# Kernel tuning notes

Hardware: AMD Instinct MI355X
Metric: run time of the kernel (lower is better)

## Reference

```python
import jax, jax.numpy as jnp
import numpy as np

N_NODES = 50000


def _gcn_layer(x, src, dst, W, b, n_nodes):
    # PyG GCNConv: h = x @ W, add self-loops, sym-normalized scatter-add, + bias
    h = x @ W  # [N, Dout]
    loop = jnp.arange(n_nodes, dtype=src.dtype)
    src2 = jnp.concatenate([src, loop])
    dst2 = jnp.concatenate([dst, loop])
    ones = jnp.ones(src2.shape[0], dtype=x.dtype)
    deg = jax.ops.segment_sum(ones, dst2, num_segments=n_nodes)  # in-degree w/ self-loops
    dinv = jnp.where(deg > 0, jax.lax.rsqrt(deg), 0.0)
    norm = dinv[src2] * dinv[dst2]  # [E+N]
    msg = h[src2] * norm[:, None]   # gather + scale
    out = jax.ops.segment_sum(msg, dst2, num_segments=n_nodes)  # scatter-add
    return out + b


def setup_inputs() -> dict:
    key = jax.random.key(0)
    k1, k2, k3, k4 = jax.random.split(key, 4)
    x = jax.random.normal(k1, (N_NODES, 128), dtype=jnp.float32)
    edge_index = jax.random.randint(k2, (2, 500000), 0, N_NODES, dtype=jnp.int64)
    W1 = jax.random.normal(k3, (128, 128), dtype=jnp.float32) * (1.0 / np.sqrt(128))
    b1 = jnp.zeros((128,), dtype=jnp.float32)
    W2 = jax.random.normal(k4, (128, 64), dtype=jnp.float32) * (1.0 / np.sqrt(128))
    b2 = jnp.zeros((64,), dtype=jnp.float32)
    return {"x": x, "edge_index": edge_index, "W1": W1, "b1": b1, "W2": W2, "b2": b2}


def reference(x, edge_index, W1, b1, W2, b2):
    src, dst = edge_index[0], edge_index[1]
    n = x.shape[0]
    h = _gcn_layer(x, src, dst, W1, b1, n)
    h = jax.nn.relu(h)
    out = _gcn_layer(h, src, dst, W2, b2, n)
    return out
```

## Files before the change

### kernel.cpp

```cpp
#include <hip/hip_runtime.h>
#include <hip/hip_bf16.h>
#include <cstddef>


typedef __attribute__((ext_vector_type(8))) short short8;
typedef __attribute__((ext_vector_type(4))) float f32x4;
typedef unsigned long long u64;

__device__ inline unsigned short f2bf(float f) {
    __hip_bfloat16 b = __float2bfloat16(f);
    return *reinterpret_cast<unsigned short*>(&b);
}
__device__ inline float bf2f_lo(unsigned int u) {
    unsigned int v = u << 16;
    return *reinterpret_cast<float*>(&v);
}
__device__ inline float bf2f_hi(unsigned int u) {
    unsigned int v = u & 0xffff0000u;
    return *reinterpret_cast<float*>(&v);
}
__device__ inline u64 ld_acq64(u64* p) {
    return __hip_atomic_load(p, __ATOMIC_ACQUIRE, __HIP_MEMORY_SCOPE_AGENT);
}
__device__ inline void st_rel64(u64* p, u64 v) {
    __hip_atomic_store(p, v, __ATOMIC_RELEASE, __HIP_MEMORY_SCOPE_AGENT);
}

__global__ __launch_bounds__(256) void count_kernel(const int* __restrict__ dst, int E,
                                                    int* __restrict__ deg,
                                                    unsigned short* __restrict__ rank,
                                                    const float* __restrict__ W1,
                                                    const float* __restrict__ W2,
                                                    unsigned short* __restrict__ W1f,
                                                    unsigned short* __restrict__ W2f,
                                                    u64* __restrict__ lb, int CB) {
    int b = blockIdx.x;
    int tid = threadIdx.x;
    if (b >= CB) {
        int idx = (b - CB) * 256 + tid;
        if (idx < 64) lb[idx] = 0;
        if (idx < 3072) {
            const float* W;
            unsigned short* Wf;
            int n, oct, Nc;
            if (idx < 2048) { W = W1; Wf = W1f; Nc = 128; n = idx >> 4; oct = idx & 15; }
            else { W = W2; Wf = W2f; Nc = 64; int i2 = idx - 2048; n = i2 >> 4; oct = i2 & 15; }
            int k0 = oct * 8;
            int ks = k0 >> 5, quad = (k0 >> 3) & 3, ntg = n >> 4;
            short8 v;
            #pragma unroll
            for (int j = 0; j < 8; j++) v[j] = (short)f2bf(W[(k0 + j) * Nc + n]);
            int off = (((ntg * 4 + ks) * 64) + (n & 15) + 16 * quad) * 8;
            *(short8*)(Wf + off) = v;
        }
        return;
    }
    int i = (b * 256 + tid) * 4;
    if (i + 3 < E) {
        int4 d = *(const int4*)(dst + i);
        unsigned short r0 = (unsigned short)atomicAdd(&deg[d.x], 1);
        unsigned short r1 = (unsigned short)atomicAdd(&deg[d.y], 1);
        unsigned short r2 = (unsigned short)atomicAdd(&deg[d.z], 1);
        unsigned short r3 = (unsigned short)atomicAdd(&deg[d.w], 1);
        *(ushort4*)(rank + i) = make_ushort4(r0, r1, r2, r3);
    } else {
        for (; i < E; i++) rank[i] = (unsigned short)atomicAdd(&deg[dst[i]], 1);
    }
}

__global__ __launch_bounds__(256) void scan_lb_kernel(const int* __restrict__ deg, int N,
                                                      u64* __restrict__ lb,
                                                      int* __restrict__ offs,
                                                      float* __restrict__ dinv) {
    __shared__ int ws[4];
    __shared__ int s_prefix;
    int tid = threadIdx.x;
    int sb = blockIdx.x;
    int SB = gridDim.x;
    int lane = tid & 63;
    int wv = tid >> 6;

    int i = sb * 1024 + tid * 4;
    int v0 = (i + 0 < N) ? deg[i + 0] : 0;
    int v1 = (i + 1 < N) ? deg[i + 1] : 0;
    int v2 = (i + 2 < N) ? deg[i + 2] : 0;
    int v3 = (i + 3 < N) ? deg[i + 3] : 0;
    int tsum = v0 + v1 + v2 + v3;
    int xs = tsum;
    #pragma unroll
    for (int off = 1; off < 64; off <<= 1) {
        int y = __shfl_up(xs, off, 64);
        if (lane >= off) xs += y;
    }
    if (lane == 63) ws[wv] = xs;
    __syncthreads();
    int wprefix = 0;
    #pragma unroll
    for (int w2 = 0; w2 < 4; w2++) wprefix += (w2 < wv) ? ws[w2] : 0;
    int chunk_total = ws[0] + ws[1] + ws[2] + ws[3];

    if (wv == 0) {
        if (lane == 0)
            st_rel64(&lb[sb], ((u64)(unsigned)chunk_total << 2) | 1ull);
        int contrib = 0;
        if (sb > 0) {
            int pred = sb - 1 - lane;
            for (;;) {
                u64 v = (pred >= 0) ? ld_acq64(&lb[pred]) : 2ull;
                int flag = (int)(v & 3);
                u64 ball2 = __ballot(flag == 2);
                u64 ball0 = __ballot(flag == 0);
                if (ball2 != 0) {
                    int L = __ffsll(ball2) - 1;
                    if ((ball0 & ((1ull << L) - 1)) == 0) {
                        contrib = (lane <= L) ? (int)(unsigned)(v >> 2) : 0;
                        break;
                    }
                }
                __builtin_amdgcn_s_sleep(1);
            }
            #pragma unroll
            for (int off = 32; off >= 1; off >>= 1)
                contrib += __shfl_xor(contrib, off, 64);
        }
        if (lane == 0) {
            st_rel64(&lb[sb], ((u64)(unsigned)(contrib + chunk_total) << 2) | 2ull);
            s_prefix = contrib;
        }
    }
    __syncthreads();

    int carry = s_prefix;
    int e0 = carry + wprefix + xs - tsum;
    int e1 = e0 + v0, e2 = e1 + v1, e3 = e2 + v2;
    if (i + 0 < N) { offs[i + 0] = e0; dinv[i + 0] = rsqrtf((float)(v0 + 1)); }
    if (i + 1 < N) { offs[i + 1] = e1; dinv[i + 1] = rsqrtf((float)(v1 + 1)); }
    if (i + 2 < N) { offs[i + 2] = e2; dinv[i + 2] = rsqrtf((float)(v2 + 1)); }
    if (i + 3 < N) { offs[i + 3] = e3; dinv[i + 3] = rsqrtf((float)(v3 + 1)); }
    if (sb == SB - 1 && tid == 0) offs[N] = carry + chunk_total;
}

__global__ __launch_bounds__(256) void fillgemm_kernel(
    const float* __restrict__ x, const unsigned short* __restrict__ W1f,
    unsigned short* __restrict__ h1, int N,
    const int* __restrict__ src, const int* __restrict__ dst, int E,
    const int* __restrict__ offs, const unsigned short* __restrict__ rank,
    const float* __restrict__ dinv, int* __restrict__ csr) {

    const int FB = (E + 255) / 256;
    int b = blockIdx.x;
    int tid = threadIdx.x;

    __shared__ unsigned short As[64 * 128];
    __shared__ float sdinv[64];

    if (b < FB) {
        int i = b * 256 + tid;
        if (i < E) {
            int s = src[i];
            int d = dst[i];
            int pos = offs[d] + (int)rank[i];
            csr[pos] = s;
        }
        return;
    }

    constexpr int K = 128, BN = 128;
    int lane = tid & 63;
    int w = tid >> 6;
    int row0 = (b - FB) * 64;

    if (tid < 64) {
        int gr = row0 + tid;
        sdinv[tid] = (gr < N) ? dinv[gr] : 0.f;
    }

    short8 bfr[2][4];
    #pragma unroll
    for (int nl = 0; nl < 2; nl++)
        #pragma unroll
        for (int ks = 0; ks < 4; ks++)
            bfr[nl][ks] = *(const short8*)(W1f + ((((w * 2 + nl) * 4 + ks) * 64) + lane) * 8);

    #pragma unroll
    for (int it = 0; it < 8; it++) {
        int idx = it * 256 + tid;
        int row = idx >> 5, kq = idx & 31;
        int k0 = kq * 4;
        int ks = k0 >> 5, quad = (k0 >> 3) & 3, j0 = k0 & 7, mt = row >> 4;
        ushort4 o = make_ushort4(0, 0, 0, 0);
        int gr = row0 + row;
        if (gr < N) {
            float4 a = *(const float4*)(x + (size_t)gr * K + k0);
            o.x = f2bf(a.x); o.y = f2bf(a.y); o.z = f2bf(a.z); o.w = f2bf(a.w);
        }
        int off = (((mt * 4 + ks) * 64) + (row & 15) + 16 * quad) * 8 + j0;
        *(ushort4*)(As + off) = o;
    }
    __syncthreads();

    f32x4 acc[4][2];
    #pragma unroll
    for (int mt = 0; mt < 4; mt++)
        #pragma unroll
        for (int nl = 0; nl < 2; nl++) acc[mt][nl] = (f32x4){0.f, 0.f, 0.f, 0.f};

    #pragma unroll
    for (int ks = 0; ks < 4; ks++) {
        short8 af[4];
        #pragma unroll
        for (int mt = 0; mt < 4; mt++)
            af[mt] = *(const short8*)(As + (((mt * 4 + ks) * 64) + lane) * 8);
        #pragma unroll
        for (int mt = 0; mt < 4; mt++)
            #pragma unroll
            for (int nl = 0; nl < 2; nl++)
                acc[mt][nl] = __builtin_amdgcn_mfma_f32_16x16x32_bf16(
                    af[mt], bfr[nl][ks], acc[mt][nl], 0, 0, 0);
    }

    int col16 = lane & 15;
    int rowq = lane >> 4;
    #pragma unroll
    for (int mt = 0; mt < 4; mt++) {
        #pragma unroll
        for (int nl = 0; nl < 2; nl++) {
            int gc = (w * 2 + nl) * 16 + col16;
            #pragma unroll
            for (int r = 0; r < 4; r++) {
                int lr = mt * 16 + rowq * 4 + r;
                int gr = row0 + lr;
                if (gr < N) h1[(size_t)gr * BN + gc] = f2bf(acc[mt][nl][r] * sdinv[lr]);
            }
        }
    }
}

__global__ __launch_bounds__(256) void aggmm_kernel(const unsigned short* __restrict__ h1,
                                                    const int* __restrict__ offs,
                                                    const int* __restrict__ csr,
                                                    const float* __restrict__ dinv,
                                                    const float* __restrict__ b1,
                                                    const unsigned short* __restrict__ W2f,
                                                    unsigned short* __restrict__ h2,
                                                    int n) {
    __shared__ unsigned short As[4 * 64 * 8];

    int tid = threadIdx.x;
    int t = tid & 63;
    int w = tid >> 6;
    int p = t >> 5;
    int t5 = t & 31;
    int nodebase = blockIdx.x * 16;
    int node0 = nodebase + w * 4;

    int ov = offs[min(node0 + min(t, 4), n)];
    int e0a[4], dega[4], cidx[4];
    #pragma unroll
    for (int i = 0; i < 4; i++) {
        e0a[i] = __shfl(ov, i, 64);
        int e1v = __shfl(ov, i + 1, 64);
        dega[i] = e1v - e0a[i];
        int ce = e0a[i] + min(t, max(dega[i] - 1, 0));
        cidx[i] = (dega[i] > 0) ? csr[ce] : 0;
    }

    short8 bw[4];
    #pragma unroll
    for (int ks = 0; ks < 4; ks++)
        bw[ks] = *(const short8*)(W2f + (((w * 4 + ks) * 64) + t) * 8);

    float4 bias = *(const float4*)(b1 + t5 * 4);

    #pragma unroll
    for (int i = 0; i < 4; i++) {
        int row16 = w * 4 + i;
        int node = node0 + i;
        float a0 = 0.f, a1 = 0.f, a2 = 0.f, a3 = 0.f;
        float di = 0.f;
        int deg = dega[i];
        int nb = min(deg, 64);
        if (node < n) {
            di = dinv[node];
            if (p == 0) {
                uint2 su = *(const uint2*)(h1 + (size_t)node * 128 + t5 * 4);
                a0 = bf2f_lo(su.x); a1 = bf2f_hi(su.x);
                a2 = bf2f_lo(su.y); a3 = bf2f_hi(su.y);
            }
            for (int jb = 0; jb < nb; jb += 8) {
                #pragma unroll
                for (int j = 0; j < 4; j++) {
                    int ee = jb + j * 2 + p;
                    int ec = min(ee, nb - 1);
                    int s = __shfl(cidx[i], ec, 64);
                    float wgt = (ee < deg) ? 1.f : 0.f;
                    uint2 hu = *(const uint2*)(h1 + (size_t)s * 128 + t5 * 4);
                    a0 += bf2f_lo(hu.x) * wgt; a1 += bf2f_hi(hu.x) * wgt;
                    a2 += bf2f_lo(hu.y) * wgt; a3 += bf2f_hi(hu.y) * wgt;
                }
            }
            int e1 = e0a[i] + deg;
            for (int eb = e0a[i] + 64; eb < e1; eb += 8) {
                #pragma unroll
                for (int j = 0; j < 4; j++) {
                    int ee = eb + j * 2 + p;
                    int ec = min(ee, e1 - 1);
                    int s = csr[ec];
                    float wgt = (ee < e1) ? 1.f : 0.f;
                    uint2 hu = *(const uint2*)(h1 + (size_t)s * 128 + t5 * 4);
                    a0 += bf2f_lo(hu.x) * wgt; a1 += bf2f_hi(hu.x) * wgt;
                    a2 += bf2f_lo(hu.y) * wgt; a3 += bf2f_hi(hu.y) * wgt;
                }
            }
        }
        a0 += __shfl_xor(a0, 32, 64);
        a1 += __shfl_xor(a1, 32, 64);
        a2 += __shfl_xor(a2, 32, 64);
        a3 += __shfl_xor(a3, 32, 64);
        if (p == 0) {
            if (node < n) {
                a0 = fmaxf(a0 * di + bias.x, 0.f);
                a1 = fmaxf(a1 * di + bias.y, 0.f);
                a2 = fmaxf(a2 * di + bias.z, 0.f);
                a3 = fmaxf(a3 * di + bias.w, 0.f);
            }
            int k0 = t5 * 4;
            int ks = k0 >> 5, quad = (k0 >> 3) & 3, j0 = k0 & 7;
            ushort4 pk4 = make_ushort4(f2bf(a0), f2bf(a1), f2bf(a2), f2bf(a3));
            *(ushort4*)(As + ((ks * 64) + row16 + 16 * quad) * 8 + j0) = pk4;
        }
    }
    __syncthreads();

    f32x4 acc = (f32x4){0.f, 0.f, 0.f, 0.f};
    #pragma unroll
    for (int ks = 0; ks < 4; ks++) {
        short8 af = *(const short8*)(As + ((ks * 64) + t) * 8);
        acc = __builtin_amdgcn_mfma_f32_16x16x32_bf16(af, bw[ks], acc, 0, 0, 0);
    }

    int col = w * 16 + (t & 15);
    int rowq = t >> 4;
    #pragma unroll
    for (int r = 0; r < 4; r++) {
        int gr = nodebase + rowq * 4 + r;
        if (gr < n) h2[(size_t)gr * 64 + col] = f2bf(acc[r] * dinv[gr]);
    }
}

__global__ __launch_bounds__(256) void aggout_kernel(const unsigned short* __restrict__ h2,
                                                     const int* __restrict__ offs,
                                                     const int* __restrict__ csr,
                                                     const float* __restrict__ dinv,
                                                     const float* __restrict__ b2,
                                                     float* __restrict__ out, int n) {
    int tid = threadIdx.x;
    int t = tid & 63;
    int w = tid >> 6;
    int node = blockIdx.x * 4 + w;
    if (node >= n) return;
    int p = t >> 4;
    int t4 = t & 15;

    int e0 = offs[node];
    int e1 = offs[node + 1];
    int deg = e1 - e0;
    int nb = min(deg, 64);
    int cidx = (deg > 0) ? csr[e0 + min(t, max(deg - 1, 0))] : 0;

    float a0 = 0.f, a1 = 0.f, a2 = 0.f, a3 = 0.f;
    float di = dinv[node];
    if (p == 0) {
        uint2 su = *(const uint2*)(h2 + (size_t)node * 64 + t4 * 4);
        a0 = bf2f_lo(su.x); a1 = bf2f_hi(su.x);
        a2 = bf2f_lo(su.y); a3 = bf2f_hi(su.y);
    }

    for (int jb = 0; jb < nb; jb += 8) {
        #pragma unroll
        for (int j = 0; j < 2; j++) {
            int ee = jb + j * 4 + p;
            int ec = min(ee, nb - 1);
            int s = __shfl(cidx, ec, 64);
            float wgt = (ee < deg) ? 1.f : 0.f;
            uint2 hu = *(const uint2*)(h2 + (size_t)s * 64 + t4 * 4);
            a0 += bf2f_lo(hu.x) * wgt; a1 += bf2f_hi(hu.x) * wgt;
            a2 += bf2f_lo(hu.y) * wgt; a3 += bf2f_hi(hu.y) * wgt;
        }
    }
    for (int eb = e0 + 64; eb < e1; eb += 8) {
        #pragma unroll
        for (int j = 0; j < 2; j++) {
            int ee = eb + j * 4 + p;
            int ec = min(ee, e1 - 1);
            int s = csr[ec];
            float wgt = (ee < e1) ? 1.f : 0.f;
            uint2 hu = *(const uint2*)(h2 + (size_t)s * 64 + t4 * 4);
            a0 += bf2f_lo(hu.x) * wgt; a1 += bf2f_hi(hu.x) * wgt;
            a2 += bf2f_lo(hu.y) * wgt; a3 += bf2f_hi(hu.y) * wgt;
        }
    }
    a0 += __shfl_xor(a0, 16, 64); a1 += __shfl_xor(a1, 16, 64);
    a2 += __shfl_xor(a2, 16, 64); a3 += __shfl_xor(a3, 16, 64);
    a0 += __shfl_xor(a0, 32, 64); a1 += __shfl_xor(a1, 32, 64);
    a2 += __shfl_xor(a2, 32, 64); a3 += __shfl_xor(a3, 32, 64);
    if (p == 0) {
        float4 bb = *(const float4*)(b2 + t4 * 4);
        *(float4*)(out + (size_t)node * 64 + t4 * 4) =
            make_float4(a0 * di + bb.x, a1 * di + bb.y, a2 * di + bb.z, a3 * di + bb.w);
    }
}

extern "C" void kernel_launch(void* const* d_in, const int* in_sizes, int n_in,
                              void* d_out, int out_size, void* d_ws, size_t ws_size,
                              hipStream_t stream) {
    const float* x  = (const float*)d_in[0];
    const int*   ei = (const int*)d_in[1];
    const float* W1 = (const float*)d_in[2];
    const float* b1 = (const float*)d_in[3];
    const float* W2 = (const float*)d_in[4];
    const float* b2 = (const float*)d_in[5];

    const int N = in_sizes[0] / 128;
    const int E = in_sizes[1] / 2;
    const int* src = ei;
    const int* dst = ei + E;

    char* p = (char*)d_ws;
    auto alloc = [&](size_t bytes) {
        char* r = p;
        p += (bytes + 255) & ~(size_t)255;
        return r;
    };
    int*   degi  = (int*)  alloc((size_t)N * 4);
    float* dinv  = (float*)alloc((size_t)N * 4);
    int*   offs  = (int*)  alloc((size_t)(N + 1) * 4);
    u64*   lb    = (u64*)  alloc((size_t)64 * 8);
    unsigned short* rank = (unsigned short*)alloc((size_t)E * 2);
    int*            csr  = (int*)alloc((size_t)E * 4);
    unsigned short* W1f  = (unsigned short*)alloc((size_t)128 * 128 * 2);
    unsigned short* W2f  = (unsigned short*)alloc((size_t)64 * 128 * 2);
    unsigned short* h1   = (unsigned short*)alloc((size_t)N * 128 * 2);
    unsigned short* h2   = (unsigned short*)alloc((size_t)N * 64 * 2);
    float* out = (float*)d_out;

    const int GB = (N + 63) / 64;
    const int FB = (E + 255) / 256;
    const int SB = (N + 1023) / 1024;
    const int CB = (E / 4 + 255) / 256;

    hipMemsetAsync(degi, 0, (size_t)N * 4, stream);
    count_kernel<<<CB + 12, 256, 0, stream>>>(dst, E, degi, rank,
                                              W1, W2, W1f, W2f, lb, CB);
    scan_lb_kernel<<<SB, 256, 0, stream>>>(degi, N, lb, offs, dinv);
    fillgemm_kernel<<<FB + GB, 256, 0, stream>>>(x, W1f, h1, N, src, dst, E,
                                                 offs, rank, dinv, csr);
    aggmm_kernel<<<(N + 15) / 16, 256, 0, stream>>>(h1, offs, csr, dinv, b1, W2f, h2, N);
    aggout_kernel<<<(N + 3) / 4, 256, 0, stream>>>(h2, offs, csr, dinv, b2, out, N);
}
```

Measured before the change: 171.2 us.

## Restructure GCN pipeline: fuse GEMM with degree count, per-edge weights, interleaved aggregation

Replaces the memset with an init kernel and moves the first GEMM into the degree-count kernel. The GEMM no longer depends on dinv, so it runs alongside the atomics instead of after the scan. The source-side normalization is now stored per edge in a csrw array written during CSR fill, and layer-1 aggregation applies it per edge. Both aggregation kernels now interleave edges from four nodes per wave to expose more memory parallelism. The cost is an extra E-sized float array plus its gather and store, and more registers per thread.

```diff
diff --git a/kernel.cpp b/kernel.cpp
--- a/kernel.cpp
+++ b/kernel.cpp
@@ -26,45 +26,127 @@
     __hip_atomic_store(p, v, __ATOMIC_RELEASE, __HIP_MEMORY_SCOPE_AGENT);
 }
 
-__global__ __launch_bounds__(256) void count_kernel(const int* __restrict__ dst, int E,
-                                                    int* __restrict__ deg,
-                                                    unsigned short* __restrict__ rank,
-                                                    const float* __restrict__ W1,
-                                                    const float* __restrict__ W2,
-                                                    unsigned short* __restrict__ W1f,
-                                                    unsigned short* __restrict__ W2f,
-                                                    u64* __restrict__ lb, int CB) {
+__global__ __launch_bounds__(256) void init_kernel(int* __restrict__ deg, int N,
+                                                   const float* __restrict__ W1,
+                                                   const float* __restrict__ W2,
+                                                   unsigned short* __restrict__ W1f,
+                                                   unsigned short* __restrict__ W2f,
+                                                   u64* __restrict__ lb, int ZB) {
     int b = blockIdx.x;
     int tid = threadIdx.x;
-    if (b >= CB) {
-        int idx = (b - CB) * 256 + tid;
-        if (idx < 64) lb[idx] = 0;
-        if (idx < 3072) {
-            const float* W;
-            unsigned short* Wf;
-            int n, oct, Nc;
-            if (idx < 2048) { W = W1; Wf = W1f; Nc = 128; n = idx >> 4; oct = idx & 15; }
-            else { W = W2; Wf = W2f; Nc = 64; int i2 = idx - 2048; n = i2 >> 4; oct = i2 & 15; }
-            int k0 = oct * 8;
-            int ks = k0 >> 5, quad = (k0 >> 3) & 3, ntg = n >> 4;
-            short8 v;
+    if (b < ZB) {
+        int i = (b * 256 + tid) * 4;
+        if (i + 3 < N) *(int4*)(deg + i) = make_int4(0, 0, 0, 0);
+        else for (; i < N; i++) deg[i] = 0;
+        return;
+    }
+    int idx = (b - ZB) * 256 + tid;
+    if (idx < 64) lb[idx] = 0;
+    if (idx < 3072) {
+        const float* W;
+        unsigned short* Wf;
+        int n, oct, Nc;
+        if (idx < 2048) { W = W1; Wf = W1f; Nc = 128; n = idx >> 4; oct = idx & 15; }
+        else { W = W2; Wf = W2f; Nc = 64; int i2 = idx - 2048; n = i2 >> 4; oct = i2 & 15; }
+        int k0 = oct * 8;
+        int ks = k0 >> 5, quad = (k0 >> 3) & 3, ntg = n >> 4;
+        short8 v;
+        #pragma unroll
+        for (int j = 0; j < 8; j++) v[j] = (short)f2bf(W[(k0 + j) * Nc + n]);
+        int off = (((ntg * 4 + ks) * 64) + (n & 15) + 16 * quad) * 8;
+        *(short8*)(Wf + off) = v;
+    }
+}
+
+__global__ __launch_bounds__(256) void countgemm_kernel(
+    const int* __restrict__ dst, int E,
+    int* __restrict__ deg, unsigned short* __restrict__ rank,
+    const float* __restrict__ x, const unsigned short* __restrict__ W1f,
+    unsigned short* __restrict__ h1, int N, int CB) {
+
+    int b = blockIdx.x;
+    int tid = threadIdx.x;
+
+    __shared__ unsigned short As[64 * 128];
+
+    if (b < CB) {
+        int i = (b * 256 + tid) * 4;
+        if (i + 3 < E) {
+            int4 d = *(const int4*)(dst + i);
+            unsigned short r0 = (unsigned short)atomicAdd(&deg[d.x], 1);
+            unsigned short r1 = (unsigned short)atomicAdd(&deg[d.y], 1);
+            unsigned short r2 = (unsigned short)atomicAdd(&deg[d.z], 1);
+            unsigned short r3 = (unsigned short)atomicAdd(&deg[d.w], 1);
+            *(ushort4*)(rank + i) = make_ushort4(r0, r1, r2, r3);
+        } else {
+            for (; i < E; i++) rank[i] = (unsigned short)atomicAdd(&deg[dst[i]], 1);
+        }
+        return;
+    }
+
+    constexpr int K = 128, BN = 128;
+    int lane = tid & 63;
+    int w = tid >> 6;
+    int row0 = (b - CB) * 64;
+
+    short8 bfr[2][4];
+    #pragma unroll
+    for (int nl = 0; nl < 2; nl++)
+        #pragma unroll
+        for (int ks = 0; ks < 4; ks++)
+            bfr[nl][ks] = *(const short8*)(W1f + ((((w * 2 + nl) * 4 + ks) * 64) + lane) * 8);
+
+    #pragma unroll
+    for (int it = 0; it < 8; it++) {
+        int idx = it * 256 + tid;
+        int row = idx >> 5, kq = idx & 31;
+        int k0 = kq * 4;
+        int ks = k0 >> 5, quad = (k0 >> 3) & 3, j0 = k0 & 7, mt = row >> 4;
+        ushort4 o = make_ushort4(0, 0, 0, 0);
+        int gr = row0 + row;
+        if (gr < N) {
+            float4 a = *(const float4*)(x + (size_t)gr * K + k0);
+            o.x = f2bf(a.x); o.y = f2bf(a.y); o.z = f2bf(a.z); o.w = f2bf(a.w);
+        }
+        int off = (((mt * 4 + ks) * 64) + (row & 15) + 16 * quad) * 8 + j0;
+        *(ushort4*)(As + off) = o;
+    }
+    __syncthreads();
+
+    f32x4 acc[4][2];
+    #pragma unroll
+    for (int mt = 0; mt < 4; mt++)
+        #pragma unroll
+        for (int nl = 0; nl < 2; nl++) acc[mt][nl] = (f32x4){0.f, 0.f, 0.f, 0.f};
+
+    #pragma unroll
+    for (int ks = 0; ks < 4; ks++) {
+        short8 af[4];
+        #pragma unroll
+        for (int mt = 0; mt < 4; mt++)
+            af[mt] = *(const short8*)(As + (((mt * 4 + ks) * 64) + lane) * 8);
+        #pragma unroll
+        for (int mt = 0; mt < 4; mt++)
             #pragma unroll
-            for (int j = 0; j < 8; j++) v[j] = (short)f2bf(W[(k0 + j) * Nc + n]);
-            int off = (((ntg * 4 + ks) * 64) + (n & 15) + 16 * quad) * 8;
-            *(short8*)(Wf + off) = v;
-        }
-        return;
-    }
-    int i = (b * 256 + tid) * 4;
-    if (i + 3 < E) {
-        int4 d = *(const int4*)(dst + i);
-        unsigned short r0 = (unsigned short)atomicAdd(&deg[d.x], 1);
-        unsigned short r1 = (unsigned short)atomicAdd(&deg[d.y], 1);
-        unsigned short r2 = (unsigned short)atomicAdd(&deg[d.z], 1);
-        unsigned short r3 = (unsigned short)atomicAdd(&deg[d.w], 1);
-        *(ushort4*)(rank + i) = make_ushort4(r0, r1, r2, r3);
-    } else {
-        for (; i < E; i++) rank[i] = (unsigned short)atomicAdd(&deg[dst[i]], 1);
+            for (int nl = 0; nl < 2; nl++)
+                acc[mt][nl] = __builtin_amdgcn_mfma_f32_16x16x32_bf16(
+                    af[mt], bfr[nl][ks], acc[mt][nl], 0, 0, 0);
+    }
+
+    int col16 = lane & 15;
+    int rowq = lane >> 4;
+    #pragma unroll
+    for (int mt = 0; mt < 4; mt++) {
+        #pragma unroll
+        for (int nl = 0; nl < 2; nl++) {
+            int gc = (w * 2 + nl) * 16 + col16;
+            #pragma unroll
+            for (int r = 0; r < 4; r++) {
+                int lr = mt * 16 + rowq * 4 + r;
+                int gr = row0 + lr;
+                if (gr < N) h1[(size_t)gr * BN + gc] = f2bf(acc[mt][nl][r]);
+            }
+        }
     }
 }
 
@@ -140,105 +222,25 @@
     if (sb == SB - 1 && tid == 0) offs[N] = carry + chunk_total;
 }
 
-__global__ __launch_bounds__(256) void fillgemm_kernel(
-    const float* __restrict__ x, const unsigned short* __restrict__ W1f,
-    unsigned short* __restrict__ h1, int N,
+__global__ __launch_bounds__(256) void fill_kernel(
     const int* __restrict__ src, const int* __restrict__ dst, int E,
     const int* __restrict__ offs, const unsigned short* __restrict__ rank,
-    const float* __restrict__ dinv, int* __restrict__ csr) {
-
-    const int FB = (E + 255) / 256;
-    int b = blockIdx.x;
-    int tid = threadIdx.x;
-
-    __shared__ unsigned short As[64 * 128];
-    __shared__ float sdinv[64];
-
-    if (b < FB) {
-        int i = b * 256 + tid;
-        if (i < E) {
-            int s = src[i];
-            int d = dst[i];
-            int pos = offs[d] + (int)rank[i];
-            csr[pos] = s;
-        }
-        return;
-    }
-
-    constexpr int K = 128, BN = 128;
-    int lane = tid & 63;
-    int w = tid >> 6;
-    int row0 = (b - FB) * 64;
-
-    if (tid < 64) {
-        int gr = row0 + tid;
-        sdinv[tid] = (gr < N) ? dinv[gr] : 0.f;
-    }
-
-    short8 bfr[2][4];
-    #pragma unroll
-    for (int nl = 0; nl < 2; nl++)
-        #pragma unroll
-        for (int ks = 0; ks < 4; ks++)
-            bfr[nl][ks] = *(const short8*)(W1f + ((((w * 2 + nl) * 4 + ks) * 64) + lane) * 8);
-
-    #pragma unroll
-    for (int it = 0; it < 8; it++) {
-        int idx = it * 256 + tid;
-        int row = idx >> 5, kq = idx & 31;
-        int k0 = kq * 4;
-        int ks = k0 >> 5, quad = (k0 >> 3) & 3, j0 = k0 & 7, mt = row >> 4;
-        ushort4 o = make_ushort4(0, 0, 0, 0);
-        int gr = row0 + row;
-        if (gr < N) {
-            float4 a = *(const float4*)(x + (size_t)gr * K + k0);
-            o.x = f2bf(a.x); o.y = f2bf(a.y); o.z = f2bf(a.z); o.w = f2bf(a.w);
-        }
-        int off = (((mt * 4 + ks) * 64) + (row & 15) + 16 * quad) * 8 + j0;
-        *(ushort4*)(As + off) = o;
-    }
-    __syncthreads();
-
-    f32x4 acc[4][2];
-    #pragma unroll
-    for (int mt = 0; mt < 4; mt++)
-        #pragma unroll
-        for (int nl = 0; nl < 2; nl++) acc[mt][nl] = (f32x4){0.f, 0.f, 0.f, 0.f};
-
-    #pragma unroll
-    for (int ks = 0; ks < 4; ks++) {
-        short8 af[4];
-        #pragma unroll
-        for (int mt = 0; mt < 4; mt++)
-            af[mt] = *(const short8*)(As + (((mt * 4 + ks) * 64) + lane) * 8);
-        #pragma unroll
-        for (int mt = 0; mt < 4; mt++)
-            #pragma unroll
-            for (int nl = 0; nl < 2; nl++)
-                acc[mt][nl] = __builtin_amdgcn_mfma_f32_16x16x32_bf16(
-                    af[mt], bfr[nl][ks], acc[mt][nl], 0, 0, 0);
-    }
-
-    int col16 = lane & 15;
-    int rowq = lane >> 4;
-    #pragma unroll
-    for (int mt = 0; mt < 4; mt++) {
-        #pragma unroll
-        for (int nl = 0; nl < 2; nl++) {
-            int gc = (w * 2 + nl) * 16 + col16;
-            #pragma unroll
-            for (int r = 0; r < 4; r++) {
-                int lr = mt * 16 + rowq * 4 + r;
-                int gr = row0 + lr;
-                if (gr < N) h1[(size_t)gr * BN + gc] = f2bf(acc[mt][nl][r] * sdinv[lr]);
-            }
-        }
+    const float* __restrict__ dinv, int* __restrict__ csr,
+    float* __restrict__ csrw) {
+    int i = blockIdx.x * 256 + threadIdx.x;
+    if (i < E) {
+        int s = src[i];
+        int d = dst[i];
+        int pos = offs[d] + (int)rank[i];
+        csr[pos] = s;
+        csrw[pos] = dinv[s];
     }
 }
 
 __global__ __launch_bounds__(256) void aggmm_kernel(const unsigned short* __restrict__ h1,
                                                     const int* __restrict__ offs,
                                                     const int* __restrict__ csr,
+                                                    const float* __restrict__ csrw,
                                                     const float* __restrict__ dinv,
                                                     const float* __restrict__ b1,
                                                     const unsigned short* __restrict__ W2f,
@@ -255,14 +257,19 @@
     int node0 = nodebase + w * 4;
 
     int ov = offs[min(node0 + min(t, 4), n)];
-    int e0a[4], dega[4], cidx[4];
+    int e0a[4], dega[4], nba[4], cidx[4];
+    float cwv[4], dia[4];
     #pragma unroll
     for (int i = 0; i < 4; i++) {
         e0a[i] = __shfl(ov, i, 64);
-        int e1v = __shfl(ov, i + 1, 64);
-        dega[i] = e1v - e0a[i];
+        dega[i] = __shfl(ov, i + 1, 64) - e0a[i];
+        nba[i] = min(dega[i], 64);
         int ce = e0a[i] + min(t, max(dega[i] - 1, 0));
-        cidx[i] = (dega[i] > 0) ? csr[ce] : 0;
+        bool has = dega[i] > 0;
+        cidx[i] = has ? csr[ce] : 0;
+        cwv[i] = has ? csrw[ce] : 0.f;
+        int node = node0 + i;
+        dia[i] = (node < n) ? dinv[node] : 0.f;
     }
 
     short8 bw[4];
@@ -272,58 +279,69 @@
 
     float4 bias = *(const float4*)(b1 + t5 * 4);
 
-    #pragma unroll
-    for (int i = 0; i < 4; i++) {
-        int row16 = w * 4 + i;
+    float a[4][4];
+    #pragma unroll
+    for (int i = 0; i < 4; i++)
+        #pragma unroll
+        for (int k = 0; k < 4; k++) a[i][k] = 0.f;
+
+    #pragma unroll
+    for (int i = 0; i < 4; i++) {
         int node = node0 + i;
-        float a0 = 0.f, a1 = 0.f, a2 = 0.f, a3 = 0.f;
-        float di = 0.f;
-        int deg = dega[i];
-        int nb = min(deg, 64);
-        if (node < n) {
-            di = dinv[node];
-            if (p == 0) {
-                uint2 su = *(const uint2*)(h1 + (size_t)node * 128 + t5 * 4);
-                a0 = bf2f_lo(su.x); a1 = bf2f_hi(su.x);
-                a2 = bf2f_lo(su.y); a3 = bf2f_hi(su.y);
-            }
-            for (int jb = 0; jb < nb; jb += 8) {
+        if (node < n && p == 0) {
+            uint2 su = *(const uint2*)(h1 + (size_t)node * 128 + t5 * 4);
+            a[i][0] = bf2f_lo(su.x) * dia[i]; a[i][1] = bf2f_hi(su.x) * dia[i];
+            a[i][2] = bf2f_lo(su.y) * dia[i]; a[i][3] = bf2f_hi(su.y) * dia[i];
+        }
+    }
+
+    int itTop = (max(max(nba[0], nba[1]), max(nba[2], nba[3])) + 3) >> 2;
+    for (int it = 0; it < itTop; ++it) {
+        int base = it * 4;
+        #pragma unroll
+        for (int i = 0; i < 4; i++) {
+            if (base < nba[i]) {
                 #pragma unroll
-                for (int j = 0; j < 4; j++) {
-                    int ee = jb + j * 2 + p;
-                    int ec = min(ee, nb - 1);
+                for (int j = 0; j < 2; j++) {
+                    int ee = base + j * 2 + p;
+                    int ec = min(ee, nba[i] - 1);
                     int s = __shfl(cidx[i], ec, 64);
-                    float wgt = (ee < deg) ? 1.f : 0.f;
+                    float wv = __shfl(cwv[i], ec, 64);
+                    wv = (ee < nba[i]) ? wv : 0.f;
                     uint2 hu = *(const uint2*)(h1 + (size_t)s * 128 + t5 * 4);
-                    a0 += bf2f_lo(hu.x) * wgt; a1 += bf2f_hi(hu.x) * wgt;
-                    a2 += bf2f_lo(hu.y) * wgt; a3 += bf2f_hi(hu.y) * wgt;
+                    a[i][0] += bf2f_lo(hu.x) * wv; a[i][1] += bf2f_hi(hu.x) * wv;
+                    a[i][2] += bf2f_lo(hu.y) * wv; a[i][3] += bf2f_hi(hu.y) * wv;
                 }
             }
-            int e1 = e0a[i] + deg;
-            for (int eb = e0a[i] + 64; eb < e1; eb += 8) {
-                #pragma unroll
-                for (int j = 0; j < 4; j++) {
-                    int ee = eb + j * 2 + p;
-                    int ec = min(ee, e1 - 1);
-                    int s = csr[ec];
-                    float wgt = (ee < e1) ? 1.f : 0.f;
-                    uint2 hu = *(const uint2*)(h1 + (size_t)s * 128 + t5 * 4);
-                    a0 += bf2f_lo(hu.x) * wgt; a1 += bf2f_hi(hu.x) * wgt;
-                    a2 += bf2f_lo(hu.y) * wgt; a3 += bf2f_hi(hu.y) * wgt;
-                }
-            }
-        }
+        }
+    }
+    #pragma unroll
+    for (int i = 0; i < 4; i++) {
+        int e1 = e0a[i] + dega[i];
+        for (int eb = e0a[i] + 64; eb < e1; eb += 2) {
+            int ee = eb + p;
+            int ec = min(ee, e1 - 1);
+            int s = csr[ec];
+            float wv = (ee < e1) ? dinv[s] : 0.f;
+            uint2 hu = *(const uint2*)(h1 + (size_t)s * 128 + t5 * 4);
+            a[i][0] += bf2f_lo(hu.x) * wv; a[i][1] += bf2f_hi(hu.x) * wv;
+            a[i][2] += bf2f_lo(hu.y) * wv; a[i][3] += bf2f_hi(hu.y) * wv;
+        }
+    }
+
+    #pragma unroll
+    for (int i = 0; i < 4; i++) {
+        float a0 = a[i][0], a1 = a[i][1], a2 = a[i][2], a3 = a[i][3];
         a0 += __shfl_xor(a0, 32, 64);
         a1 += __shfl_xor(a1, 32, 64);
         a2 += __shfl_xor(a2, 32, 64);
         a3 += __shfl_xor(a3, 32, 64);
         if (p == 0) {
-            if (node < n) {
-                a0 = fmaxf(a0 * di + bias.x, 0.f);
-                a1 = fmaxf(a1 * di + bias.y, 0.f);
-                a2 = fmaxf(a2 * di + bias.z, 0.f);
-                a3 = fmaxf(a3 * di + bias.w, 0.f);
-            }
+            a0 = fmaxf(a0 * dia[i] + bias.x, 0.f);
+            a1 = fmaxf(a1 * dia[i] + bias.y, 0.f);
+            a2 = fmaxf(a2 * dia[i] + bias.z, 0.f);
+            a3 = fmaxf(a3 * dia[i] + bias.w, 0.f);
+            int row16 = w * 4 + i;
             int k0 = t5 * 4;
             int ks = k0 >> 5, quad = (k0 >> 3) & 3, j0 = k0 & 7;
             ushort4 pk4 = make_ushort4(f2bf(a0), f2bf(a1), f2bf(a2), f2bf(a3));
@@ -357,57 +375,84 @@
     int tid = threadIdx.x;
     int t = tid & 63;
     int w = tid >> 6;
-    int node = blockIdx.x * 4 + w;
-    if (node >= n) return;
     int p = t >> 4;
     int t4 = t & 15;
-
-    int e0 = offs[node];
-    int e1 = offs[node + 1];
-    int deg = e1 - e0;
-    int nb = min(deg, 64);
-    int cidx = (deg > 0) ? csr[e0 + min(t, max(deg - 1, 0))] : 0;
-
-    float a0 = 0.f, a1 = 0.f, a2 = 0.f, a3 = 0.f;
-    float di = dinv[node];
-    if (p == 0) {
-        uint2 su = *(const uint2*)(h2 + (size_t)node * 64 + t4 * 4);
-        a0 = bf2f_lo(su.x); a1 = bf2f_hi(su.x);
-        a2 = bf2f_lo(su.y); a3 = bf2f_hi(su.y);
-    }
-
-    for (int jb = 0; jb < nb; jb += 8) {
-        #pragma unroll
-        for (int j = 0; j < 2; j++) {
-            int ee = jb + j * 4 + p;
-            int ec = min(ee, nb - 1);
-            int s = __shfl(cidx, ec, 64);
-            float wgt = (ee < deg) ? 1.f : 0.f;
-            uint2 hu = *(const uint2*)(h2 + (size_t)s * 64 + t4 * 4);
-            a0 += bf2f_lo(hu.x) * wgt; a1 += bf2f_hi(hu.x) * wgt;
-            a2 += bf2f_lo(hu.y) * wgt; a3 += bf2f_hi(hu.y) * wgt;
-        }
-    }
-    for (int eb = e0 + 64; eb < e1; eb += 8) {
-        #pragma unroll
-        for (int j = 0; j < 2; j++) {
-            int ee = eb + j * 4 + p;
+    int node0 = blockIdx.x * 16 + w * 4;
+
+    int ov = offs[min(node0 + min(t, 4), n)];
+    int e0a[4], dega[4], nba[4], cidx[4];
+    float dia[4];
+    #pragma unroll
+    for (int i = 0; i < 4; i++) {
+        e0a[i] = __shfl(ov, i, 64);
+        dega[i] = __shfl(ov, i + 1, 64) - e0a[i];
+        nba[i] = min(dega[i], 64);
+        int ce = e0a[i] + min(t, max(dega[i] - 1, 0));
+        cidx[i] = (dega[i] > 0) ? csr[ce] : 0;
+        int node = node0 + i;
+        dia[i] = (node < n) ? dinv[node] : 0.f;
+    }
+
+    float a[4][4];
+    #pragma unroll
+    for (int i = 0; i < 4; i++)
+        #pragma unroll
+        for (int k = 0; k < 4; k++) a[i][k] = 0.f;
+
+    #pragma unroll
+    for (int i = 0; i < 4; i++) {
+        int node = node0 + i;
+        if (node < n && p == 0) {
+            uint2 su = *(const uint2*)(h2 + (size_t)node * 64 + t4 * 4);
+            a[i][0] = bf2f_lo(su.x); a[i][1] = bf2f_hi(su.x);
+            a[i][2] = bf2f_lo(su.y); a[i][3] = bf2f_hi(su.y);
+        }
+    }
+
+    int itTop = (max(max(nba[0], nba[1]), max(nba[2], nba[3])) + 3) >> 2;
+    for (int it = 0; it < itTop; ++it) {
+        int base = it * 4;
+        #pragma unroll
+        for (int i = 0; i < 4; i++) {
+            if (base < nba[i]) {
+                int ee = base + p;
+                int ec = min(ee, nba[i] - 1);
+                int s = __shfl(cidx[i], ec, 64);
+                float wgt = (ee < nba[i]) ? 1.f : 0.f;
+                uint2 hu = *(const uint2*)(h2 + (size_t)s * 64 + t4 * 4);
+                a[i][0] += bf2f_lo(hu.x) * wgt; a[i][1] += bf2f_hi(hu.x) * wgt;
+                a[i][2] += bf2f_lo(hu.y) * wgt; a[i][3] += bf2f_hi(hu.y) * wgt;
+            }
+        }
+    }
+    #pragma unroll
+    for (int i = 0; i < 4; i++) {
+        int e1 = e0a[i] + dega[i];
+        for (int eb = e0a[i] + 64; eb < e1; eb += 4) {
+            int ee = eb + p;
             int ec = min(ee, e1 - 1);
             int s = csr[ec];
             float wgt = (ee < e1) ? 1.f : 0.f;
             uint2 hu = *(const uint2*)(h2 + (size_t)s * 64 + t4 * 4);
-            a0 += bf2f_lo(hu.x) * wgt; a1 += bf2f_hi(hu.x) * wgt;
-            a2 += bf2f_lo(hu.y) * wgt; a3 += bf2f_hi(hu.y) * wgt;
-        }
-    }
-    a0 += __shfl_xor(a0, 16, 64); a1 += __shfl_xor(a1, 16, 64);
-    a2 += __shfl_xor(a2, 16, 64); a3 += __shfl_xor(a3, 16, 64);
-    a0 += __shfl_xor(a0, 32, 64); a1 += __shfl_xor(a1, 32, 64);
-    a2 += __shfl_xor(a2, 32, 64); a3 += __shfl_xor(a3, 32, 64);
-    if (p == 0) {
-        float4 bb = *(const float4*)(b2 + t4 * 4);
-        *(float4*)(out + (size_t)node * 64 + t4 * 4) =
-            make_float4(a0 * di + bb.x, a1 * di + bb.y, a2 * di + bb.z, a3 * di + bb.w);
+            a[i][0] += bf2f_lo(hu.x) * wgt; a[i][1] += bf2f_hi(hu.x) * wgt;
+            a[i][2] += bf2f_lo(hu.y) * wgt; a[i][3] += bf2f_hi(hu.y) * wgt;
+        }
+    }
+
+    #pragma unroll
+    for (int i = 0; i < 4; i++) {
+        float a0 = a[i][0], a1 = a[i][1], a2 = a[i][2], a3 = a[i][3];
+        a0 += __shfl_xor(a0, 16, 64); a1 += __shfl_xor(a1, 16, 64);
+        a2 += __shfl_xor(a2, 16, 64); a3 += __shfl_xor(a3, 16, 64);
+        a0 += __shfl_xor(a0, 32, 64); a1 += __shfl_xor(a1, 32, 64);
+        a2 += __shfl_xor(a2, 32, 64); a3 += __shfl_xor(a3, 32, 64);
+        int node = node0 + i;
+        if (p == 0 && node < n) {
+            float4 bb = *(const float4*)(b2 + t4 * 4);
+            *(float4*)(out + (size_t)node * 64 + t4 * 4) =
+                make_float4(a0 * dia[i] + bb.x, a1 * dia[i] + bb.y,
+                            a2 * dia[i] + bb.z, a3 * dia[i] + bb.w);
+        }
     }
 }
 
@@ -438,6 +483,7 @@
     u64*   lb    = (u64*)  alloc((size_t)64 * 8);
     unsigned short* rank = (unsigned short*)alloc((size_t)E * 2);
     int*            csr  = (int*)alloc((size_t)E * 4);
+    float*          csrw = (float*)alloc((size_t)E * 4);
     unsigned short* W1f  = (unsigned short*)alloc((size_t)128 * 128 * 2);
     unsigned short* W2f  = (unsigned short*)alloc((size_t)64 * 128 * 2);
     unsigned short* h1   = (unsigned short*)alloc((size_t)N * 128 * 2);
@@ -448,13 +494,12 @@
     const int FB = (E + 255) / 256;
     const int SB = (N + 1023) / 1024;
     const int CB = (E / 4 + 255) / 256;
-
-    hipMemsetAsync(degi, 0, (size_t)N * 4, stream);
-    count_kernel<<<CB + 12, 256, 0, stream>>>(dst, E, degi, rank,
-                                              W1, W2, W1f, W2f, lb, CB);
+    const int ZB = (N + 1023) / 1024;
+
+    init_kernel<<<ZB + 12, 256, 0, stream>>>(degi, N, W1, W2, W1f, W2f, lb, ZB);
+    countgemm_kernel<<<CB + GB, 256, 0, stream>>>(dst, E, degi, rank, x, W1f, h1, N, CB);
     scan_lb_kernel<<<SB, 256, 0, stream>>>(degi, N, lb, offs, dinv);
-    fillgemm_kernel<<<FB + GB, 256, 0, stream>>>(x, W1f, h1, N, src, dst, E,
-                                                 offs, rank, dinv, csr);
-    aggmm_kernel<<<(N + 15) / 16, 256, 0, stream>>>(h1, offs, csr, dinv, b1, W2f, h2, N);
-    aggout_kernel<<<(N + 3) / 4, 256, 0, stream>>>(h2, offs, csr, dinv, b2, out, N);
-}
+    fill_kernel<<<FB, 256, 0, stream>>>(src, dst, E, offs, rank, dinv, csr, csrw);
+    aggmm_kernel<<<(N + 15) / 16, 256, 0, stream>>>(h1, offs, csr, csrw, dinv, b1, W2f, h2, N);
+    aggout_kernel<<<(N + 15) / 16, 256, 0, stream>>>(h2, offs, csr, dinv, b2, out, N);
+}
```

Measured after the change: 190.6 us. 11.3% more time.

## Split gather aggregation into 32-feature column chunks with 8 edges per wave step

Applied to the files above, without the earlier changes.

Both aggregation kernels now loop over 32-column feature chunks, with 8 lanes covering a chunk and 8 edges gathered in parallel per step, instead of 32 or 16 lanes covering the full row. aggout now handles 4 nodes per wave (16 per block) like aggmm, so the launch grid shrinks. The aim is to shorten the serial edge loop for typical degrees near 11 and to amortise the offset and index loads across nodes. In exchange, each neighbor row is gathered in several separate chunk passes, which may hurt locality, and there are more shuffle reductions per node.

```diff
diff --git a/kernel.cpp b/kernel.cpp
--- a/kernel.cpp
+++ b/kernel.cpp
@@ -249,20 +249,23 @@
     int tid = threadIdx.x;
     int t = tid & 63;
     int w = tid >> 6;
-    int p = t >> 5;
-    int t5 = t & 31;
+    int p8 = t >> 3;
+    int q = t & 7;
     int nodebase = blockIdx.x * 16;
     int node0 = nodebase + w * 4;
 
     int ov = offs[min(node0 + min(t, 4), n)];
-    int e0a[4], dega[4], cidx[4];
+    int e0a[4], dega[4], nba[4], cidx[4];
+    float dia[4];
     #pragma unroll
     for (int i = 0; i < 4; i++) {
         e0a[i] = __shfl(ov, i, 64);
-        int e1v = __shfl(ov, i + 1, 64);
-        dega[i] = e1v - e0a[i];
+        dega[i] = __shfl(ov, i + 1, 64) - e0a[i];
+        nba[i] = min(dega[i], 64);
         int ce = e0a[i] + min(t, max(dega[i] - 1, 0));
         cidx[i] = (dega[i] > 0) ? csr[ce] : 0;
+        int node = node0 + i;
+        dia[i] = (node < n) ? dinv[node] : 0.f;
     }
 
     short8 bw[4];
@@ -270,64 +273,56 @@
     for (int ks = 0; ks < 4; ks++)
         bw[ks] = *(const short8*)(W2f + (((w * 4 + ks) * 64) + t) * 8);
 
-    float4 bias = *(const float4*)(b1 + t5 * 4);
-
-    #pragma unroll
-    for (int i = 0; i < 4; i++) {
-        int row16 = w * 4 + i;
-        int node = node0 + i;
-        float a0 = 0.f, a1 = 0.f, a2 = 0.f, a3 = 0.f;
-        float di = 0.f;
-        int deg = dega[i];
-        int nb = min(deg, 64);
-        if (node < n) {
-            di = dinv[node];
-            if (p == 0) {
-                uint2 su = *(const uint2*)(h1 + (size_t)node * 128 + t5 * 4);
-                a0 = bf2f_lo(su.x); a1 = bf2f_hi(su.x);
-                a2 = bf2f_lo(su.y); a3 = bf2f_hi(su.y);
-            }
-            for (int jb = 0; jb < nb; jb += 8) {
-                #pragma unroll
-                for (int j = 0; j < 4; j++) {
-                    int ee = jb + j * 2 + p;
-                    int ec = min(ee, nb - 1);
+    #pragma unroll
+    for (int c = 0; c < 4; c++) {
+        float4 bias = *(const float4*)(b1 + c * 32 + q * 4);
+        #pragma unroll
+        for (int i = 0; i < 4; i++) {
+            int node = node0 + i;
+            float a0 = 0.f, a1 = 0.f, a2 = 0.f, a3 = 0.f;
+            if (node < n) {
+                if (p8 == 0) {
+                    uint2 su = *(const uint2*)(h1 + (size_t)node * 128 + c * 32 + q * 4);
+                    a0 = bf2f_lo(su.x); a1 = bf2f_hi(su.x);
+                    a2 = bf2f_lo(su.y); a3 = bf2f_hi(su.y);
+                }
+                for (int jb = 0; jb < nba[i]; jb += 8) {
+                    int ee = jb + p8;
+                    int ec = min(ee, nba[i] - 1);
                     int s = __shfl(cidx[i], ec, 64);
-                    float wgt = (ee < deg) ? 1.f : 0.f;
-                    uint2 hu = *(const uint2*)(h1 + (size_t)s * 128 + t5 * 4);
+                    float wgt = (ee < nba[i]) ? 1.f : 0.f;
+                    uint2 hu = *(const uint2*)(h1 + (size_t)s * 128 + c * 32 + q * 4);
                     a0 += bf2f_lo(hu.x) * wgt; a1 += bf2f_hi(hu.x) * wgt;
                     a2 += bf2f_lo(hu.y) * wgt; a3 += bf2f_hi(hu.y) * wgt;
                 }
-            }
-            int e1 = e0a[i] + deg;
-            for (int eb = e0a[i] + 64; eb < e1; eb += 8) {
-                #pragma unroll
-                for (int j = 0; j < 4; j++) {
-                    int ee = eb + j * 2 + p;
+                int e1 = e0a[i] + dega[i];
+                for (int eb = e0a[i] + 64; eb < e1; eb += 8) {
+                    int ee = eb + p8;
                     int ec = min(ee, e1 - 1);
                     int s = csr[ec];
                     float wgt = (ee < e1) ? 1.f : 0.f;
-                    uint2 hu = *(const uint2*)(h1 + (size_t)s * 128 + t5 * 4);
+                    uint2 hu = *(const uint2*)(h1 + (size_t)s * 128 + c * 32 + q * 4);
                     a0 += bf2f_lo(hu.x) * wgt; a1 += bf2f_hi(hu.x) * wgt;
                     a2 += bf2f_lo(hu.y) * wgt; a3 += bf2f_hi(hu.y) * wgt;
                 }
             }
-        }
-        a0 += __shfl_xor(a0, 32, 64);
-        a1 += __shfl_xor(a1, 32, 64);
-        a2 += __shfl_xor(a2, 32, 64);
-        a3 += __shfl_xor(a3, 32, 64);
-        if (p == 0) {
-            if (node < n) {
-                a0 = fmaxf(a0 * di + bias.x, 0.f);
-                a1 = fmaxf(a1 * di + bias.y, 0.f);
-                a2 = fmaxf(a2 * di + bias.z, 0.f);
-                a3 = fmaxf(a3 * di + bias.w, 0.f);
-            }
-            int k0 = t5 * 4;
-            int ks = k0 >> 5, quad = (k0 >> 3) & 3, j0 = k0 & 7;
-            ushort4 pk4 = make_ushort4(f2bf(a0), f2bf(a1), f2bf(a2), f2bf(a3));
-            *(ushort4*)(As + ((ks * 64) + row16 + 16 * quad) * 8 + j0) = pk4;
+            a0 += __shfl_xor(a0, 8, 64);  a1 += __shfl_xor(a1, 8, 64);
+            a2 += __shfl_xor(a2, 8, 64);  a3 += __shfl_xor(a3, 8, 64);
+            a0 += __shfl_xor(a0, 16, 64); a1 += __shfl_xor(a1, 16, 64);
+            a2 += __shfl_xor(a2, 16, 64); a3 += __shfl_xor(a3, 16, 64);
+            a0 += __shfl_xor(a0, 32, 64); a1 += __shfl_xor(a1, 32, 64);
+            a2 += __shfl_xor(a2, 32, 64); a3 += __shfl_xor(a3, 32, 64);
+            if (p8 == 0) {
+                a0 = fmaxf(a0 * dia[i] + bias.x, 0.f);
+                a1 = fmaxf(a1 * dia[i] + bias.y, 0.f);
+                a2 = fmaxf(a2 * dia[i] + bias.z, 0.f);
+                a3 = fmaxf(a3 * dia[i] + bias.w, 0.f);
+                int row16 = w * 4 + i;
+                int k0 = c * 32 + q * 4;
+                int ks = k0 >> 5, quad = (k0 >> 3) & 3, j0 = k0 & 7;
+                ushort4 pk4 = make_ushort4(f2bf(a0), f2bf(a1), f2bf(a2), f2bf(a3));
+                *(ushort4*)(As + ((ks * 64) + row16 + 16 * quad) * 8 + j0) = pk4;
+            }
         }
     }
     __syncthreads();
@@ -357,57 +352,69 @@
     int tid = threadIdx.x;
     int t = tid & 63;
     int w = tid >> 6;
-    int node = blockIdx.x * 4 + w;
-    if (node >= n) return;
-    int p = t >> 4;
-    int t4 = t & 15;
-
-    int e0 = offs[node];
-    int e1 = offs[node + 1];
-    int deg = e1 - e0;
-    int nb = min(deg, 64);
-    int cidx = (deg > 0) ? csr[e0 + min(t, max(deg - 1, 0))] : 0;
-
-    float a0 = 0.f, a1 = 0.f, a2 = 0.f, a3 = 0.f;
-    float di = dinv[node];
-    if (p == 0) {
-        uint2 su = *(const uint2*)(h2 + (size_t)node * 64 + t4 * 4);
-        a0 = bf2f_lo(su.x); a1 = bf2f_hi(su.x);
-        a2 = bf2f_lo(su.y); a3 = bf2f_hi(su.y);
-    }
-
-    for (int jb = 0; jb < nb; jb += 8) {
-        #pragma unroll
-        for (int j = 0; j < 2; j++) {
-            int ee = jb + j * 4 + p;
-            int ec = min(ee, nb - 1);
-            int s = __shfl(cidx, ec, 64);
-            float wgt = (ee < deg) ? 1.f : 0.f;
-            uint2 hu = *(const uint2*)(h2 + (size_t)s * 64 + t4 * 4);
-            a0 += bf2f_lo(hu.x) * wgt; a1 += bf2f_hi(hu.x) * wgt;
-            a2 += bf2f_lo(hu.y) * wgt; a3 += bf2f_hi(hu.y) * wgt;
-        }
-    }
-    for (int eb = e0 + 64; eb < e1; eb += 8) {
-        #pragma unroll
-        for (int j = 0; j < 2; j++) {
-            int ee = eb + j * 4 + p;
-            int ec = min(ee, e1 - 1);
-            int s = csr[ec];
-            float wgt = (ee < e1) ? 1.f : 0.f;
-            uint2 hu = *(const uint2*)(h2 + (size_t)s * 64 + t4 * 4);
-            a0 += bf2f_lo(hu.x) * wgt; a1 += bf2f_hi(hu.x) * wgt;
-            a2 += bf2f_lo(hu.y) * wgt; a3 += bf2f_hi(hu.y) * wgt;
-        }
-    }
-    a0 += __shfl_xor(a0, 16, 64); a1 += __shfl_xor(a1, 16, 64);
-    a2 += __shfl_xor(a2, 16, 64); a3 += __shfl_xor(a3, 16, 64);
-    a0 += __shfl_xor(a0, 32, 64); a1 += __shfl_xor(a1, 32, 64);
-    a2 += __shfl_xor(a2, 32, 64); a3 += __shfl_xor(a3, 32, 64);
-    if (p == 0) {
-        float4 bb = *(const float4*)(b2 + t4 * 4);
-        *(float4*)(out + (size_t)node * 64 + t4 * 4) =
-            make_float4(a0 * di + bb.x, a1 * di + bb.y, a2 * di + bb.z, a3 * di + bb.w);
+    int p8 = t >> 3;
+    int q = t & 7;
+    int node0 = blockIdx.x * 16 + w * 4;
+
+    int ov = offs[min(node0 + min(t, 4), n)];
+    int e0a[4], dega[4], nba[4], cidx[4];
+    float dia[4];
+    #pragma unroll
+    for (int i = 0; i < 4; i++) {
+        e0a[i] = __shfl(ov, i, 64);
+        dega[i] = __shfl(ov, i + 1, 64) - e0a[i];
+        nba[i] = min(dega[i], 64);
+        int ce = e0a[i] + min(t, max(dega[i] - 1, 0));
+        cidx[i] = (dega[i] > 0) ? csr[ce] : 0;
+        int node = node0 + i;
+        dia[i] = (node < n) ? dinv[node] : 0.f;
+    }
+
+    #pragma unroll
+    for (int c = 0; c < 2; c++) {
+        float4 bb = *(const float4*)(b2 + c * 32 + q * 4);
+        #pragma unroll
+        for (int i = 0; i < 4; i++) {
+            int node = node0 + i;
+            float a0 = 0.f, a1 = 0.f, a2 = 0.f, a3 = 0.f;
+            if (node < n) {
+                if (p8 == 0) {
+                    uint2 su = *(const uint2*)(h2 + (size_t)node * 64 + c * 32 + q * 4);
+                    a0 = bf2f_lo(su.x); a1 = bf2f_hi(su.x);
+                    a2 = bf2f_lo(su.y); a3 = bf2f_hi(su.y);
+                }
+                for (int jb = 0; jb < nba[i]; jb += 8) {
+                    int ee = jb + p8;
+                    int ec = min(ee, nba[i] - 1);
+                    int s = __shfl(cidx[i], ec, 64);
+                    float wgt = (ee < nba[i]) ? 1.f : 0.f;
+                    uint2 hu = *(const uint2*)(h2 + (size_t)s * 64 + c * 32 + q * 4);
+                    a0 += bf2f_lo(hu.x) * wgt; a1 += bf2f_hi(hu.x) * wgt;
+                    a2 += bf2f_lo(hu.y) * wgt; a3 += bf2f_hi(hu.y) * wgt;
+                }
+                int e1 = e0a[i] + dega[i];
+                for (int eb = e0a[i] + 64; eb < e1; eb += 8) {
+                    int ee = eb + p8;
+                    int ec = min(ee, e1 - 1);
+                    int s = csr[ec];
+                    float wgt = (ee < e1) ? 1.f : 0.f;
+                    uint2 hu = *(const uint2*)(h2 + (size_t)s * 64 + c * 32 + q * 4);
+                    a0 += bf2f_lo(hu.x) * wgt; a1 += bf2f_hi(hu.x) * wgt;
+                    a2 += bf2f_lo(hu.y) * wgt; a3 += bf2f_hi(hu.y) * wgt;
+                }
+            }
+            a0 += __shfl_xor(a0, 8, 64);  a1 += __shfl_xor(a1, 8, 64);
+            a2 += __shfl_xor(a2, 8, 64);  a3 += __shfl_xor(a3, 8, 64);
+            a0 += __shfl_xor(a0, 16, 64); a1 += __shfl_xor(a1, 16, 64);
+            a2 += __shfl_xor(a2, 16, 64); a3 += __shfl_xor(a3, 16, 64);
+            a0 += __shfl_xor(a0, 32, 64); a1 += __shfl_xor(a1, 32, 64);
+            a2 += __shfl_xor(a2, 32, 64); a3 += __shfl_xor(a3, 32, 64);
+            if (p8 == 0 && node < n) {
+                *(float4*)(out + (size_t)node * 64 + c * 32 + q * 4) =
+                    make_float4(a0 * dia[i] + bb.x, a1 * dia[i] + bb.y,
+                                a2 * dia[i] + bb.z, a3 * dia[i] + bb.w);
+            }
+        }
     }
 }
 
@@ -456,5 +463,5 @@
     fillgemm_kernel<<<FB + GB, 256, 0, stream>>>(x, W1f, h1, N, src, dst, E,
                                                  offs, rank, dinv, csr);
     aggmm_kernel<<<(N + 15) / 16, 256, 0, stream>>>(h1, offs, csr, dinv, b1, W2f, h2, N);
-    aggout_kernel<<<(N + 3) / 4, 256, 0, stream>>>(h2, offs, csr, dinv, b2, out, N);
-}
+    aggout_kernel<<<(N + 15) / 16, 256, 0, stream>>>(h2, offs, csr, dinv, b2, out, N);
+}
```

Measured after the change: 215.7 us. 1.26x slower.
